# Optimization experiments

Hardware: AMD Instinct MI355X
Metric: run time of the kernel (lower is better)

Reference implementation:

```python
import jax, jax.numpy as jnp
import numpy as np

IN_FEATURES = 4096
OUT_FEATURES = 11008
B, S = 4, 2048


def setup_inputs() -> dict:
    key = jax.random.key(0)
    k1, k2, k3, k4 = jax.random.split(key, 4)
    x = jax.random.normal(k1, (B, S, IN_FEATURES), dtype=jnp.float32)
    # int8 quantized weights in [-127, 127]
    weight_quantized = jax.random.randint(k2, (OUT_FEATURES, IN_FEATURES), -127, 128, dtype=jnp.int8)
    # realistic per-channel scales (positive, small)
    weight_scale = jax.random.uniform(k3, (OUT_FEATURES,), dtype=jnp.float32, minval=1e-4, maxval=2e-2)
    bias = jax.random.normal(k4, (OUT_FEATURES,), dtype=jnp.float32) * 0.01
    return {"x": x, "weight_quantized": weight_quantized, "weight_scale": weight_scale, "bias": bias}


def reference(x, weight_quantized, weight_scale, bias):
    # Dequantize: W = int8.float() * scale[:, None]  (symmetric, per-channel)
    w = weight_quantized.astype(jnp.float32) * weight_scale[:, None]  # [out, in]
    # F.linear: y = x @ W^T + b
    return jnp.einsum('bsi,oi->bso', x, w) + bias
```

## Files before the change

kernel.cpp:

```cpp
#include <hip/hip_runtime.h>
#include <hip/hip_bf16.h>
#include <stdint.h>


#define M_TOTAL 8192
#define K_TOTAL 4096
#define N_TOTAL 11008
#define NT 32
#define NBM 32
#define NBN 43

typedef __attribute__((ext_vector_type(4))) int int4v;


__global__ __launch_bounds__(256) void quant_x_kernel(const float* __restrict__ x,
                                                      signed char* __restrict__ xq,
                                                      float* __restrict__ sx) {
    const int row = blockIdx.x;
    const int tid = threadIdx.x;
    const float* xr = x + (size_t)row * K_TOTAL + tid * 16;

    float4 v0 = reinterpret_cast<const float4*>(xr)[0];
    float4 v1 = reinterpret_cast<const float4*>(xr)[1];
    float4 v2 = reinterpret_cast<const float4*>(xr)[2];
    float4 v3 = reinterpret_cast<const float4*>(xr)[3];

    float m = 0.f;
    m = fmaxf(m, fmaxf(fmaxf(fabsf(v0.x), fabsf(v0.y)), fmaxf(fabsf(v0.z), fabsf(v0.w))));
    m = fmaxf(m, fmaxf(fmaxf(fabsf(v1.x), fabsf(v1.y)), fmaxf(fabsf(v1.z), fabsf(v1.w))));
    m = fmaxf(m, fmaxf(fmaxf(fabsf(v2.x), fabsf(v2.y)), fmaxf(fabsf(v2.z), fabsf(v2.w))));
    m = fmaxf(m, fmaxf(fmaxf(fabsf(v3.x), fabsf(v3.y)), fmaxf(fabsf(v3.z), fabsf(v3.w))));

    for (int d = 1; d < 64; d <<= 1) m = fmaxf(m, __shfl_xor(m, d));
    __shared__ float wm_[4];
    if ((tid & 63) == 0) wm_[tid >> 6] = m;
    __syncthreads();
    m = fmaxf(fmaxf(wm_[0], wm_[1]), fmaxf(wm_[2], wm_[3]));

    const float inv = (m > 0.f) ? (127.f / m) : 0.f;
    if (tid == 0) sx[row] = (m > 0.f) ? (m / 127.f) : 0.f;

    float tmp[16] = {v0.x,v0.y,v0.z,v0.w, v1.x,v1.y,v1.z,v1.w,
                     v2.x,v2.y,v2.z,v2.w, v3.x,v3.y,v3.z,v3.w};
    int q[16];
#pragma unroll
    for (int i = 0; i < 16; ++i) {
        int t = __float2int_rn(tmp[i] * inv);
        q[i] = t > 127 ? 127 : (t < -127 ? -127 : t);
    }
    int4v o;
#pragma unroll
    for (int w = 0; w < 4; ++w)
        o[w] = (q[w*4] & 255) | ((q[w*4+1] & 255) << 8) |
               ((q[w*4+2] & 255) << 16) | ((q[w*4+3] & 255) << 24);
    *reinterpret_cast<int4v*>(xq + (size_t)row * K_TOTAL + tid * 16) = o;
}


__global__ __launch_bounds__(256) void cvt_w_kernel(const int* __restrict__ in,
                                                    signed char* __restrict__ out, int nitems) {
    bool is8 = false;
    for (int i = 0; i < 256; ++i) {
        int v = in[i];
        if (v < -127 || v > 127) { is8 = true; break; }
    }
    int stride = gridDim.x * blockDim.x;
    if (!is8) {
        for (int i = blockIdx.x * blockDim.x + threadIdx.x; i < nitems; i += stride) {
            const int* p = in + (size_t)i * 16;
            int4v o;
#pragma unroll
            for (int w = 0; w < 4; ++w)
                o[w] = (p[w*4] & 255) | ((p[w*4+1] & 255) << 8) |
                       ((p[w*4+2] & 255) << 16) | ((p[w*4+3] & 255) << 24);
            *reinterpret_cast<int4v*>(out + (size_t)i * 16) = o;
        }
    } else {
        const int4v* in16 = reinterpret_cast<const int4v*>(in);
        for (int i = blockIdx.x * blockDim.x + threadIdx.x; i < nitems; i += stride)
            *reinterpret_cast<int4v*>(out + (size_t)i * 16) = in16[i];
    }
}


#define GLOAD16(g, l) __builtin_amdgcn_global_load_lds( \
    (const __attribute__((address_space(1))) void*)(g), \
    (__attribute__((address_space(3))) void*)(l), 16, 0, 0)


#define RD_A8(dst, base, KX)                                                    \
    _Pragma("unroll")                                                           \
    for (int i_ = 0; i_ < 8; ++i_)                                              \
        dst[i_] = *(const int4v*)((base) + (wm * 128 + i_ * 16 + fr) * 128 + (KX));
#define RD_B4(dst, base, KX)                                                    \
    _Pragma("unroll")                                                           \
    for (int n_ = 0; n_ < 4; ++n_)                                              \
        dst[n_] = *(const int4v*)((base) + 32768 + (wn * 64 + n_ * 16 + fr) * 128 + (KX));
#define MFMA32(fa, fb)                                                          \
    __builtin_amdgcn_s_setprio(1);                                              \
    _Pragma("unroll")                                                           \
    for (int i_ = 0; i_ < 8; ++i_) {                                            \
        _Pragma("unroll")                                                       \
        for (int n_ = 0; n_ < 4; ++n_)                                          \
            acc[i_][n_] = __builtin_amdgcn_mfma_i32_16x16x64_i8(                \
                fa[i_], fb[n_], acc[i_][n_], 0, 0, 0);                          \
    }                                                                           \
    __builtin_amdgcn_s_setprio(0);
#define STAGE_A(asrc, buf)                                                      \
    _Pragma("unroll")                                                           \
    for (int i_ = 0; i_ < 4; ++i_)                                              \
        GLOAD16((asrc) + soff[i_], (buf) + (c0 + i_) * 1024);
#define STAGE_B(bsrc, buf)                                                      \
    _Pragma("unroll")                                                           \
    for (int i_ = 0; i_ < 4; ++i_)                                              \
        GLOAD16((bsrc) + soff[i_], (buf) + 32768 + (c0 + i_) * 1024);

__global__ __launch_bounds__(512, 2) void gemm_kernel(const unsigned char* __restrict__ A,
                                                      const unsigned char* __restrict__ B,
                                                      const float* __restrict__ sx,
                                                      const float* __restrict__ scale,
                                                      const float* __restrict__ bias,
                                                      float* __restrict__ C) {
    __shared__ unsigned char sh[131072];

    const int tid  = threadIdx.x;
    const int wv   = tid >> 6;
    const int lane = tid & 63;
    const int wm   = wv >> 2;
    const int wn   = wv & 3;

    const int xcd = blockIdx.x & 7;
    const int l   = blockIdx.x >> 3;
    const int bm  = xcd * 4 + (l & 3);
    const int bn  = l >> 2;

    const int fr  = lane & 15;
    const int fq  = lane >> 4;
    const int swz = fr & 7;
    const int kx0 = (fq ^ swz) * 16;
    const int kx1 = ((4 + fq) ^ swz) * 16;

    const int c0 = wv * 4;
    const int rl = lane >> 3;
    const int sg = (lane & 7) ^ rl;
    int soff[4];
#pragma unroll
    for (int i = 0; i < 4; ++i)
        soff[i] = ((c0 + i) * 8 + rl) * K_TOTAL + sg * 16;

    const unsigned char* aS = A + (size_t)bm * 256 * K_TOTAL;
    const unsigned char* bS = B + (size_t)bn * 256 * K_TOTAL;
    unsigned char* buf0 = sh;
    unsigned char* buf1 = sh + 65536;

    int4v acc[8][4] = {};
    int4v afX[8], afY[8], bf0v[4], bf1v[4];

    STAGE_A(aS, buf0)
    STAGE_B(bS, buf0)
    STAGE_B(bS + 128, buf1)
    asm volatile("s_waitcnt vmcnt(4)" ::: "memory");
    __builtin_amdgcn_s_barrier();
    RD_A8(afX, buf0, kx0)
    RD_B4(bf0v, buf0, kx0)
    RD_B4(bf1v, buf0, kx1)

#pragma unroll 1
    for (int t = 0; t < NT; ++t) {
        const int p = t & 1;
        unsigned char* bp = p ? buf1 : buf0;
        unsigned char* bq = p ? buf0 : buf1;

        RD_A8(afY, bp, kx1)
        if (t + 1 < NT) { STAGE_A(aS + (size_t)(t + 1) * 128, bq) }
        MFMA32(afX, bf0v)
        asm volatile("s_waitcnt lgkmcnt(0)" ::: "memory");
        __builtin_amdgcn_s_barrier();

        if (t + 2 < NT) { STAGE_B(bS + (size_t)(t + 2) * 128, bp) }
        MFMA32(afY, bf1v)
        if (t + 1 < NT) {
            if (t + 2 < NT) { asm volatile("s_waitcnt vmcnt(4)" ::: "memory"); }
            else            { asm volatile("s_waitcnt vmcnt(0)" ::: "memory"); }
        }
        __builtin_amdgcn_s_barrier();
        if (t + 1 < NT) {
            RD_A8(afX, bq, kx0)
            RD_B4(bf0v, bq, kx0)
            RD_B4(bf1v, bq, kx1)
        }
    }

    const int crow0 = bm * 256 + wm * 128;
    const int ccol0 = bn * 256 + wn * 64;
    float scv[4], bsv[4];
#pragma unroll
    for (int n = 0; n < 4; ++n) {
        const int col = ccol0 + n * 16 + fr;
        scv[n] = scale[col];
        bsv[n] = bias[col];
    }
#pragma unroll
    for (int fm = 0; fm < 8; ++fm) {
#pragma unroll
        for (int j = 0; j < 4; ++j) {
            const int row = crow0 + fm * 16 + fq * 4 + j;
            const float sr = sx[row];
            float* cp = C + (size_t)row * N_TOTAL + ccol0 + fr;
#pragma unroll
            for (int n = 0; n < 4; ++n)
                cp[n * 16] = (float)acc[fm][n][j] * (sr * scv[n]) + bsv[n];
        }
    }
}


__global__ __launch_bounds__(256) void gemm_fallback(const float* __restrict__ x,
                                                     const int* __restrict__ w,
                                                     const float* __restrict__ scale,
                                                     const float* __restrict__ bias,
                                                     float* __restrict__ C) {
    bool is8 = false;
    for (int i = 0; i < 256; ++i) {
        int v = w[i];
        if (v < -127 || v > 127) { is8 = true; break; }
    }
    const signed char* w8 = (const signed char*)w;

    __shared__ float As[64][16];
    __shared__ float Bs[64][16];
    const int nbn = N_TOTAL / 64;
    const int bm = blockIdx.x / nbn;
    const int bn = blockIdx.x % nbn;
    const int tid = threadIdx.x;
    const int tx = tid & 15, ty = tid >> 4;

    float acc[4][4] = {};
    for (int kt = 0; kt < K_TOTAL; kt += 16) {
        for (int i = 0; i < 4; ++i) {
            int idx = tid + i * 256;
            int rr = idx >> 4, cc = idx & 15;
            As[rr][cc] = x[(size_t)(bm * 64 + rr) * K_TOTAL + kt + cc];
            size_t widx = (size_t)(bn * 64 + rr) * K_TOTAL + kt + cc;
            Bs[rr][cc] = is8 ? (float)w8[widx] : (float)w[widx];
        }
        __syncthreads();
        for (int kk = 0; kk < 16; ++kk) {
            float a[4], b[4];
            for (int i = 0; i < 4; ++i) a[i] = As[ty * 4 + i][kk];
            for (int j = 0; j < 4; ++j) b[j] = Bs[tx * 4 + j][kk];
            for (int i = 0; i < 4; ++i)
                for (int j = 0; j < 4; ++j) acc[i][j] += a[i] * b[j];
        }
        __syncthreads();
    }
    for (int j = 0; j < 4; ++j) {
        int col = bn * 64 + tx * 4 + j;
        float s = scale[col], bb = bias[col];
        for (int i = 0; i < 4; ++i) {
            int row = bm * 64 + ty * 4 + i;
            C[(size_t)row * N_TOTAL + col] = acc[i][j] * s + bb;
        }
    }
}


extern "C" void kernel_launch(void* const* d_in, const int* in_sizes, int n_in,
                              void* d_out, int out_size, void* d_ws, size_t ws_size,
                              hipStream_t stream) {
    const float* x     = (const float*)d_in[0];
    const int*   wq    = (const int*)d_in[1];
    const float* scale = (const float*)d_in[2];
    const float* bias  = (const float*)d_in[3];
    float*       out   = (float*)d_out;

    const size_t x_bytes = (size_t)M_TOTAL * K_TOTAL;
    const size_t w_bytes = (size_t)N_TOTAL * K_TOTAL;
    const size_t need = x_bytes + w_bytes + M_TOTAL * sizeof(float);

    if (ws_size >= need) {
        signed char* xq = (signed char*)d_ws;
        signed char* wb = (signed char*)d_ws + x_bytes;
        float*       sx = (float*)((char*)d_ws + x_bytes + w_bytes);

        quant_x_kernel<<<M_TOTAL, 256, 0, stream>>>(x, xq, sx);
        cvt_w_kernel<<<2048, 256, 0, stream>>>(wq, wb, (int)(w_bytes / 16));
        dim3 grid(NBM * NBN);
        gemm_kernel<<<grid, 512, 0, stream>>>((const unsigned char*)xq,
                                              (const unsigned char*)wb,
                                              sx, scale, bias, out);
    } else {
        dim3 grid((M_TOTAL / 64) * (N_TOTAL / 64));
        gemm_fallback<<<grid, 256, 0, stream>>>(x, wq, scale, bias, out);
    }
}
```

Measured before the change: 462.5 us.

## Simplify GEMM main loop to a plain double-buffered tile pipeline

Replaces the staggered A/B prefetch schedule with a simple double-buffered loop. Each tile issues the global loads for the next tile, reads all LDS fragments, runs both MFMA groups, then waits for all outstanding loads and barriers. This cuts register pressure and schedule complexity. In exchange it loses the split barriers and the overlap of LDS reads with MFMA, and a full vmcnt(0) per tile may expose global load latency.

```diff
diff --git a/kernel.cpp b/kernel.cpp
--- a/kernel.cpp
+++ b/kernel.cpp
@@ -115,6 +115,23 @@
     for (int i_ = 0; i_ < 4; ++i_)                                              \
         GLOAD16((bsrc) + soff[i_], (buf) + 32768 + (c0 + i_) * 1024);
 
+#define TILE(bp, bq, tnext)                                                     \
+    {                                                                           \
+        if ((tnext) < NT) {                                                     \
+            STAGE_A(aS + (size_t)(tnext) * 128, bq)                             \
+            STAGE_B(bS + (size_t)(tnext) * 128, bq)                             \
+        }                                                                       \
+        int4v afX[8], afY[8], bf0v[4], bf1v[4];                                 \
+        RD_A8(afX, bp, kx0)                                                     \
+        RD_B4(bf0v, bp, kx0)                                                    \
+        RD_A8(afY, bp, kx1)                                                     \
+        RD_B4(bf1v, bp, kx1)                                                    \
+        MFMA32(afX, bf0v)                                                       \
+        MFMA32(afY, bf1v)                                                       \
+        asm volatile("s_waitcnt lgkmcnt(0) vmcnt(0)" ::: "memory");             \
+        __builtin_amdgcn_s_barrier();                                           \
+    }
+
 __global__ __launch_bounds__(512, 2) void gemm_kernel(const unsigned char* __restrict__ A,
                                                       const unsigned char* __restrict__ B,
                                                       const float* __restrict__ sx,
@@ -154,41 +171,16 @@
     unsigned char* buf1 = sh + 65536;
 
     int4v acc[8][4] = {};
-    int4v afX[8], afY[8], bf0v[4], bf1v[4];
 
     STAGE_A(aS, buf0)
     STAGE_B(bS, buf0)
-    STAGE_B(bS + 128, buf1)
-    asm volatile("s_waitcnt vmcnt(4)" ::: "memory");
+    asm volatile("s_waitcnt vmcnt(0)" ::: "memory");
     __builtin_amdgcn_s_barrier();
-    RD_A8(afX, buf0, kx0)
-    RD_B4(bf0v, buf0, kx0)
-    RD_B4(bf1v, buf0, kx1)
 
 #pragma unroll 1
-    for (int t = 0; t < NT; ++t) {
-        const int p = t & 1;
-        unsigned char* bp = p ? buf1 : buf0;
-        unsigned char* bq = p ? buf0 : buf1;
-
-        RD_A8(afY, bp, kx1)
-        if (t + 1 < NT) { STAGE_A(aS + (size_t)(t + 1) * 128, bq) }
-        MFMA32(afX, bf0v)
-        asm volatile("s_waitcnt lgkmcnt(0)" ::: "memory");
-        __builtin_amdgcn_s_barrier();
-
-        if (t + 2 < NT) { STAGE_B(bS + (size_t)(t + 2) * 128, bp) }
-        MFMA32(afY, bf1v)
-        if (t + 1 < NT) {
-            if (t + 2 < NT) { asm volatile("s_waitcnt vmcnt(4)" ::: "memory"); }
-            else            { asm volatile("s_waitcnt vmcnt(0)" ::: "memory"); }
-        }
-        __builtin_amdgcn_s_barrier();
-        if (t + 1 < NT) {
-            RD_A8(afX, bq, kx0)
-            RD_B4(bf0v, bq, kx0)
-            RD_B4(bf1v, bq, kx1)
-        }
+    for (int u = 0; u < NT / 2; ++u) {
+        TILE(buf0, buf1, 2 * u + 1)
+        TILE(buf1, buf0, 2 * u + 2)
     }
 
     const int crow0 = bm * 256 + wm * 128;
```

Result: slower. 965.8 us (+108.8%).

## Load LDS fragments in-iteration and interleave with grouped MFMA via sched barriers

Applied to the files above, without the earlier changes.

Drops the cross-barrier register prefetch of A/B fragments for the next tile. Each half-iteration now reads its fragments from the current LDS buffer and then runs the MFMAs in four row groups separated by scheduling barriers. The aim is to cut register pressure and let fine-grained LDS waits overlap with the first MFMA groups. The cost is that LDS read latency now sits at the start of each half-iteration instead of being hidden behind the previous tile's compute.

```diff
diff --git a/kernel.cpp b/kernel.cpp
--- a/kernel.cpp
+++ b/kernel.cpp
@@ -96,10 +96,10 @@
     _Pragma("unroll")                                                           \
     for (int n_ = 0; n_ < 4; ++n_)                                              \
         dst[n_] = *(const int4v*)((base) + 32768 + (wn * 64 + n_ * 16 + fr) * 128 + (KX));
-#define MFMA32(fa, fb)                                                          \
+#define MFMA_G(fa, fb, g)                                                       \
     __builtin_amdgcn_s_setprio(1);                                              \
     _Pragma("unroll")                                                           \
-    for (int i_ = 0; i_ < 8; ++i_) {                                            \
+    for (int i_ = 2*(g); i_ < 2*(g)+2; ++i_) {                                  \
         _Pragma("unroll")                                                       \
         for (int n_ = 0; n_ < 4; ++n_)                                          \
             acc[i_][n_] = __builtin_amdgcn_mfma_i32_16x16x64_i8(                \
@@ -114,6 +114,7 @@
     _Pragma("unroll")                                                           \
     for (int i_ = 0; i_ < 4; ++i_)                                              \
         GLOAD16((bsrc) + soff[i_], (buf) + 32768 + (c0 + i_) * 1024);
+#define SB __builtin_amdgcn_sched_barrier(0)
 
 __global__ __launch_bounds__(512, 2) void gemm_kernel(const unsigned char* __restrict__ A,
                                                       const unsigned char* __restrict__ B,
@@ -154,16 +155,12 @@
     unsigned char* buf1 = sh + 65536;
 
     int4v acc[8][4] = {};
-    int4v afX[8], afY[8], bf0v[4], bf1v[4];
 
     STAGE_A(aS, buf0)
     STAGE_B(bS, buf0)
     STAGE_B(bS + 128, buf1)
     asm volatile("s_waitcnt vmcnt(4)" ::: "memory");
     __builtin_amdgcn_s_barrier();
-    RD_A8(afX, buf0, kx0)
-    RD_B4(bf0v, buf0, kx0)
-    RD_B4(bf1v, buf0, kx1)
 
 #pragma unroll 1
     for (int t = 0; t < NT; ++t) {
@@ -171,24 +168,39 @@
         unsigned char* bp = p ? buf1 : buf0;
         unsigned char* bq = p ? buf0 : buf1;
 
-        RD_A8(afY, bp, kx1)
+        int4v afX[8], afY[8], bf0v[4], bf1v[4];
+
         if (t + 1 < NT) { STAGE_A(aS + (size_t)(t + 1) * 128, bq) }
-        MFMA32(afX, bf0v)
+        RD_B4(bf0v, bp, kx0)
+        RD_B4(bf1v, bp, kx1)
+        RD_A8(afX, bp, kx0)
+        SB;
+        MFMA_G(afX, bf0v, 0)
+        SB;
+        MFMA_G(afX, bf0v, 1)
+        SB;
+        MFMA_G(afX, bf0v, 2)
+        SB;
+        MFMA_G(afX, bf0v, 3)
         asm volatile("s_waitcnt lgkmcnt(0)" ::: "memory");
         __builtin_amdgcn_s_barrier();
 
         if (t + 2 < NT) { STAGE_B(bS + (size_t)(t + 2) * 128, bp) }
-        MFMA32(afY, bf1v)
+        RD_A8(afY, bp, kx1)
+        SB;
+        MFMA_G(afY, bf1v, 0)
+        SB;
+        MFMA_G(afY, bf1v, 1)
+        SB;
+        MFMA_G(afY, bf1v, 2)
+        SB;
+        MFMA_G(afY, bf1v, 3)
+        asm volatile("s_waitcnt lgkmcnt(0)" ::: "memory");
         if (t + 1 < NT) {
             if (t + 2 < NT) { asm volatile("s_waitcnt vmcnt(4)" ::: "memory"); }
             else            { asm volatile("s_waitcnt vmcnt(0)" ::: "memory"); }
         }
         __builtin_amdgcn_s_barrier();
-        if (t + 1 < NT) {
-            RD_A8(afX, bq, kx0)
-            RD_B4(bf0v, bq, kx0)
-            RD_B4(bf1v, bq, kx1)
-        }
     }
 
     const int crow0 = bm * 256 + wm * 128;
```

Result: no change. 466.8 us (+0.9%).
